# Performance work log

Hardware: AMD Instinct MI355X
Metric: run time of the kernel (lower is better)

## Reference

```python
import jax, jax.numpy as jnp
import numpy as np


def setup_inputs() -> dict:
    key = jax.random.key(0)
    kq, kk, kv = jax.random.split(key, 3)
    B, H, S, D = 2, 8, 2048, 64
    Q = jax.random.normal(kq, (B, H, S, D), dtype=jnp.float32)
    K = jax.random.normal(kk, (B, 1, S, D), dtype=jnp.float32)
    V = jax.random.normal(kv, (B, 1, S, D), dtype=jnp.float32)
    return {"Q": Q, "K": K, "V": V}


def reference(Q, K, V):
    # Multi-query attention: K/V have a single shared head.
    D = Q.shape[-1]
    scale = 1.0 / jnp.sqrt(jnp.asarray(D, dtype=Q.dtype))
    Kh = K[:, 0]  # [B, S, D]
    Vh = V[:, 0]  # [B, S, D]
    # scores: [B, H, Sq, Sk]
    scores = jnp.einsum('bhqd,bkd->bhqk', Q, Kh) * scale
    probs = jax.nn.softmax(scores, axis=-1)
    out = jnp.einsum('bhqk,bkd->bhqd', probs, Vh)  # [B, H, S, D]
    return out
```

## Files before the change

kernel.cpp:

```cpp
#include <hip/hip_runtime.h>
#include <hip/hip_bf16.h>
#include <stdint.h>

typedef __attribute__((ext_vector_type(8)))  short    bf16x8;
typedef __attribute__((ext_vector_type(16))) float    f32x16;
typedef __attribute__((ext_vector_type(2)))  float    f32x2;
typedef __attribute__((ext_vector_type(4)))  float    float4v;
typedef __attribute__((ext_vector_type(4)))  unsigned uint4v;
typedef __attribute__((ext_vector_type(2)))  int      int2v;

#define DEVINL static __device__ __forceinline__

#define B_  2
#define H_  8
#define S_  2048
#define D_  64
#define KVB 128
#define NKT (S_ / KVB)

DEVINL unsigned short f2bf(float f) {
  union { float f; unsigned u; } v; v.f = f;
  unsigned r = v.u + 0x7FFFu + ((v.u >> 16) & 1u);
  return (unsigned short)(r >> 16);
}

DEVINL unsigned short bfu(float f) {
  __hip_bfloat16 h = __float2bfloat16(f);
  unsigned short u; __builtin_memcpy(&u, &h, 2); return u;
}

DEVINL unsigned pkcvt(float a, float b) {
  return (unsigned)bfu(a) | ((unsigned)bfu(b) << 16);
}

DEVINL void gload_lds16(const void* g, void* l) {
  __builtin_amdgcn_global_load_lds(
      (const __attribute__((address_space(1))) void*)g,
      (__attribute__((address_space(3))) void*)l, 16, 0, 0);
}

DEVINL bf16x8 frag_from_words(unsigned a, unsigned b, unsigned c, unsigned d) {
  union { unsigned u[4]; bf16x8 v; } x;
  x.u[0] = a; x.u[1] = b; x.u[2] = c; x.u[3] = d;
  return x.v;
}

#define CROW(r, hi) (((r) & 3) + 8 * ((r) >> 2) + 4 * (hi))

__global__ __launch_bounds__(256) void prep_kernel(
    const float* __restrict__ K, const float* __restrict__ V,
    unsigned short* __restrict__ KVf) {
  const int blk = blockIdx.x;
  const int b  = blk >> 5;
  const int kt = (blk >> 1) & 15;
  const int t  = threadIdx.x;
  const int w  = t >> 6, l = t & 63;
  const int lq = l & 31, hi = l >> 5;

  unsigned short* out = KVf + (size_t)(b * 16 + kt) * 16384;

  if ((blk & 1) == 0) {
#pragma unroll
    for (int j = 0; j < 4; ++j) {
      const int fi = w * 4 + j;
      const int kh = fi >> 2, ks = fi & 3;
      const float* src = K + ((size_t)(b * 2048 + kt * 128 + kh * 32 + lq)) * 64 + ks * 16 + hi * 8;
      const float4v x0 = *(const float4v*)(src);
      const float4v x1 = *(const float4v*)(src + 4);
      uint4v o;
      o.x = (unsigned)f2bf(x0.x) | ((unsigned)f2bf(x0.y) << 16);
      o.y = (unsigned)f2bf(x0.z) | ((unsigned)f2bf(x0.w) << 16);
      o.z = (unsigned)f2bf(x1.x) | ((unsigned)f2bf(x1.y) << 16);
      o.w = (unsigned)f2bf(x1.z) | ((unsigned)f2bf(x1.w) << 16);
      *(uint4v*)(out + fi * 512 + l * 8) = o;
    }
  } else {
    __shared__ float Vs[128][65];
#pragma unroll
    for (int rep = 0; rep < 4; ++rep) {
      const int row = rep * 32 + (t >> 3);
      const int col = (t & 7) * 8;
      const float* src = V + ((size_t)(b * 2048 + kt * 128 + row)) * 64 + col;
      const float4v y0 = *(const float4v*)(src);
      const float4v y1 = *(const float4v*)(src + 4);
      Vs[row][col + 0] = y0.x; Vs[row][col + 1] = y0.y;
      Vs[row][col + 2] = y0.z; Vs[row][col + 3] = y0.w;
      Vs[row][col + 4] = y1.x; Vs[row][col + 5] = y1.y;
      Vs[row][col + 6] = y1.z; Vs[row][col + 7] = y1.w;
    }
    __syncthreads();
#pragma unroll
    for (int j = 0; j < 4; ++j) {
      const int fj = w * 4 + j;
      const int kh = fj >> 2, s = (fj >> 1) & 1, nt = fj & 1;
      const int d  = nt * 32 + lq;
      const int k0 = kh * 32 + s * 16 + hi * 8;
      unsigned short o[8];
#pragma unroll
      for (int e = 0; e < 8; ++e) o[e] = f2bf(Vs[k0 + e][d]);
      uint4v wv;
      wv.x = (unsigned)o[0] | ((unsigned)o[1] << 16);
      wv.y = (unsigned)o[2] | ((unsigned)o[3] << 16);
      wv.z = (unsigned)o[4] | ((unsigned)o[5] << 16);
      wv.w = (unsigned)o[6] | ((unsigned)o[7] << 16);
      *(uint4v*)(out + (16 + fj) * 512 + l * 8) = wv;
    }
  }
}

__global__ __launch_bounds__(512, 4) void attn_kernel(
    const float* __restrict__ Q, const unsigned short* __restrict__ KVf,
    float* __restrict__ O) {
  __shared__ __align__(16) unsigned char smem[65536];

  const int bid = blockIdx.x;
  const int b  = bid >> 8;
  const int h  = (bid >> 5) & 7;
  const int qt = bid & 31;

  const int tid  = threadIdx.x;
  const int lane = tid & 63;
  const int wave = tid >> 6;
  const int qg   = wave & 1;
  const int kh   = wave >> 1;
  const int hi   = lane >> 5;
  const int lq   = lane & 31;

  const unsigned char* kp = (const unsigned char*)KVf + (size_t)b * 16 * 32768;

  const float qscale = 0.125f * 1.4426950408889634f;
  const float* qrow = Q + ((size_t)((b * H_ + h) * S_) + (size_t)(qt * 64 + qg * 32 + lq)) * 64;
  bf16x8 qfrag[4];
#pragma unroll
  for (int ks = 0; ks < 4; ++ks) {
    const float* p = qrow + ks * 16 + hi * 8;
    float4v x0 = *(const float4v*)(p);
    float4v x1 = *(const float4v*)(p + 4);
    bf16x8 f;
    f[0] = (short)f2bf(x0.x * qscale); f[1] = (short)f2bf(x0.y * qscale);
    f[2] = (short)f2bf(x0.z * qscale); f[3] = (short)f2bf(x0.w * qscale);
    f[4] = (short)f2bf(x1.x * qscale); f[5] = (short)f2bf(x1.y * qscale);
    f[6] = (short)f2bf(x1.z * qscale); f[7] = (short)f2bf(x1.w * qscale);
    qfrag[ks] = f;
  }

  f32x16 acc0, acc1;
#pragma unroll
  for (int r = 0; r < 16; ++r) { acc0[r] = 0.f; acc1[r] = 0.f; }
  float lrun = 0.f;

#define STAGE(BUF)                                                        \
  do {                                                                    \
    _Pragma("unroll")                                                     \
    for (int j = 0; j < 4; ++j)                                           \
      gload_lds16(kp + j * 8192 + tid * 16,                               \
                  smem + (BUF) * 32768 + j * 8192 + tid * 16);            \
    kp += 32768;                                                          \
  } while (0)

  STAGE(0);

  int buf = 0;
  for (int kt = 0; kt < NKT; ++kt) {
    __syncthreads();

    if (kt + 1 < NKT) STAGE(buf ^ 1);

    const unsigned short* Kt = (const unsigned short*)(smem + buf * 32768) + kh * 2048;
    f32x16 c;
#pragma unroll
    for (int r = 0; r < 16; ++r) c[r] = 0.f;
    __builtin_amdgcn_s_setprio(1);
#pragma unroll
    for (int ks = 0; ks < 4; ++ks) {
      const bf16x8 a = *(const bf16x8*)(Kt + ks * 512 + lane * 8);
      c = __builtin_amdgcn_mfma_f32_32x32x16_bf16(a, qfrag[ks], c, 0, 0, 0);
    }
    __builtin_amdgcn_s_setprio(0);

#pragma unroll
    for (int r = 0; r < 16; ++r) c[r] = __builtin_amdgcn_exp2f(c[r]);
    f32x2 ps = (f32x2){0.f, 0.f};
#pragma unroll
    for (int r = 0; r < 8; ++r) ps += (f32x2){c[2 * r], c[2 * r + 1]};
    lrun += ps.x + ps.y;

    const unsigned short* Vt = (const unsigned short*)(smem + buf * 32768) + 8192 + kh * 2048;
#pragma unroll
    for (int s = 0; s < 2; ++s) {
      const unsigned wx0 = pkcvt(c[8 * s + 0], c[8 * s + 1]);
      const unsigned wx1 = pkcvt(c[8 * s + 2], c[8 * s + 3]);
      const unsigned wy0 = pkcvt(c[8 * s + 4], c[8 * s + 5]);
      const unsigned wy1 = pkcvt(c[8 * s + 6], c[8 * s + 7]);
      const int2v s02 = __builtin_amdgcn_permlane32_swap((int)wx0, (int)wy0, false, false);
      const int2v s13 = __builtin_amdgcn_permlane32_swap((int)wx1, (int)wy1, false, false);
      const bf16x8 pfrag = frag_from_words((unsigned)s02.x, (unsigned)s13.x,
                                           (unsigned)s02.y, (unsigned)s13.y);
      __builtin_amdgcn_s_setprio(1);
      const bf16x8 bv0 = *(const bf16x8*)(Vt + (s * 2 + 0) * 512 + lane * 8);
      acc0 = __builtin_amdgcn_mfma_f32_32x32x16_bf16(pfrag, bv0, acc0, 0, 0, 0);
      const bf16x8 bv1 = *(const bf16x8*)(Vt + (s * 2 + 1) * 512 + lane * 8);
      acc1 = __builtin_amdgcn_mfma_f32_32x32x16_bf16(pfrag, bv1, acc1, 0, 0, 0);
      __builtin_amdgcn_s_setprio(0);
    }

    buf ^= 1;
  }

  const float lfull = lrun + __shfl_xor(lrun, 32);
  __syncthreads();
  float* Lb = (float*)smem;
  float* Ab = Lb + 256;
  if (lane < 32) Lb[(qg * 4 + kh) * 32 + lane] = lfull;
  __syncthreads();
  const float ltot = Lb[(qg * 4 + 0) * 32 + lq] + Lb[(qg * 4 + 1) * 32 + lq]
                   + Lb[(qg * 4 + 2) * 32 + lq] + Lb[(qg * 4 + 3) * 32 + lq];

  if (kh > 0) {
    float* dst = Ab + (size_t)(qg * 3 + (kh - 1)) * 2048;
#pragma unroll
    for (int r = 0; r < 16; ++r) {
      dst[CROW(r, hi) * 64 + lq]      = acc0[r];
      dst[CROW(r, hi) * 64 + 32 + lq] = acc1[r];
    }
  }
  __syncthreads();
  if (kh == 0) {
    const float linv = 1.f / ltot;
    const float* a0 = Ab + (size_t)(qg * 3 + 0) * 2048;
    const float* a1 = Ab + (size_t)(qg * 3 + 1) * 2048;
    const float* a2 = Ab + (size_t)(qg * 3 + 2) * 2048;
    float* obase = O + ((size_t)((b * H_ + h) * S_) + (size_t)(qt * 64 + qg * 32)) * 64;
#pragma unroll
    for (int r = 0; r < 16; ++r) {
      const float iv = __shfl(linv, CROW(r, hi));
      const int row  = CROW(r, hi);
      obase[(size_t)row * 64 + lq] =
          (acc0[r] + a0[row * 64 + lq] + a1[row * 64 + lq] + a2[row * 64 + lq]) * iv;
      obase[(size_t)row * 64 + 32 + lq] =
          (acc1[r] + a0[row * 64 + 32 + lq] + a1[row * 64 + 32 + lq] + a2[row * 64 + 32 + lq]) * iv;
    }
  }
}

extern "C" void kernel_launch(void* const* d_in, const int* in_sizes, int n_in,
                              void* d_out, int out_size, void* d_ws, size_t ws_size,
                              hipStream_t stream) {
  const float* Q = (const float*)d_in[0];
  const float* K = (const float*)d_in[1];
  const float* V = (const float*)d_in[2];
  float* O = (float*)d_out;

  unsigned short* KVf = (unsigned short*)d_ws;

  prep_kernel<<<64, 256, 0, stream>>>(K, V, KVf);
  attn_kernel<<<B_ * H_ * (S_ / 64), 512, 0, stream>>>(Q, KVf, O);
}
```

Measured before the change: 38.57 us.

## Use 4 waves per block, each handling both query groups, with barrier-free per-wave staging

Cuts the block from 8 waves to 4. Each wave now computes both 32-row query groups against its own K/V slice, so every K and V fragment read from LDS is reused for two MFMA chains. Each wave stages only its own slice of LDS via direct global-to-LDS loads and waits with vmcnt instead of a block-wide __syncthreads per tile, which removes per-iteration barriers. In exchange each wave holds twice the accumulators and Q fragments, which raises register pressure, and there are fewer waves per block to hide latency.

Result: no change. 39.25 us (+1.8%).

```diff
diff --git a/kernel.cpp b/kernel.cpp
--- a/kernel.cpp
+++ b/kernel.cpp
@@ -108,7 +108,7 @@
   }
 }
 
-__global__ __launch_bounds__(512, 4) void attn_kernel(
+__global__ __launch_bounds__(256, 2) void attn_kernel(
     const float* __restrict__ Q, const unsigned short* __restrict__ KVf,
     float* __restrict__ O) {
   __shared__ __align__(16) unsigned char smem[65536];
@@ -120,125 +120,178 @@
 
   const int tid  = threadIdx.x;
   const int lane = tid & 63;
-  const int wave = tid >> 6;
-  const int qg   = wave & 1;
-  const int kh   = wave >> 1;
+  const int kh   = tid >> 6;
   const int hi   = lane >> 5;
   const int lq   = lane & 31;
 
-  const unsigned char* kp = (const unsigned char*)KVf + (size_t)b * 16 * 32768;
+  const unsigned char* wsrc = (const unsigned char*)KVf
+      + (size_t)b * 16 * 32768 + (size_t)kh * 4096 + (size_t)lane * 16;
+  unsigned char* wdst = smem + (size_t)kh * 4096 + (size_t)lane * 16;
 
   const float qscale = 0.125f * 1.4426950408889634f;
-  const float* qrow = Q + ((size_t)((b * H_ + h) * S_) + (size_t)(qt * 64 + qg * 32 + lq)) * 64;
-  bf16x8 qfrag[4];
-#pragma unroll
-  for (int ks = 0; ks < 4; ++ks) {
-    const float* p = qrow + ks * 16 + hi * 8;
-    float4v x0 = *(const float4v*)(p);
-    float4v x1 = *(const float4v*)(p + 4);
-    bf16x8 f;
-    f[0] = (short)f2bf(x0.x * qscale); f[1] = (short)f2bf(x0.y * qscale);
-    f[2] = (short)f2bf(x0.z * qscale); f[3] = (short)f2bf(x0.w * qscale);
-    f[4] = (short)f2bf(x1.x * qscale); f[5] = (short)f2bf(x1.y * qscale);
-    f[6] = (short)f2bf(x1.z * qscale); f[7] = (short)f2bf(x1.w * qscale);
-    qfrag[ks] = f;
-  }
-
-  f32x16 acc0, acc1;
-#pragma unroll
-  for (int r = 0; r < 16; ++r) { acc0[r] = 0.f; acc1[r] = 0.f; }
-  float lrun = 0.f;
-
-#define STAGE(BUF)                                                        \
-  do {                                                                    \
-    _Pragma("unroll")                                                     \
-    for (int j = 0; j < 4; ++j)                                           \
-      gload_lds16(kp + j * 8192 + tid * 16,                               \
-                  smem + (BUF) * 32768 + j * 8192 + tid * 16);            \
-    kp += 32768;                                                          \
+  bf16x8 qfrag0[4], qfrag1[4];
+#pragma unroll
+  for (int qg = 0; qg < 2; ++qg) {
+    const float* qrow = Q + ((size_t)((b * H_ + h) * S_) + (size_t)(qt * 64 + qg * 32 + lq)) * 64;
+#pragma unroll
+    for (int ks = 0; ks < 4; ++ks) {
+      const float* p = qrow + ks * 16 + hi * 8;
+      float4v x0 = *(const float4v*)(p);
+      float4v x1 = *(const float4v*)(p + 4);
+      bf16x8 f;
+      f[0] = (short)f2bf(x0.x * qscale); f[1] = (short)f2bf(x0.y * qscale);
+      f[2] = (short)f2bf(x0.z * qscale); f[3] = (short)f2bf(x0.w * qscale);
+      f[4] = (short)f2bf(x1.x * qscale); f[5] = (short)f2bf(x1.y * qscale);
+      f[6] = (short)f2bf(x1.z * qscale); f[7] = (short)f2bf(x1.w * qscale);
+      if (qg == 0) qfrag0[ks] = f; else qfrag1[ks] = f;
+    }
+  }
+
+  f32x16 acc00, acc01, acc10, acc11;
+#pragma unroll
+  for (int r = 0; r < 16; ++r) { acc00[r] = 0.f; acc01[r] = 0.f; acc10[r] = 0.f; acc11[r] = 0.f; }
+  float lrun0 = 0.f, lrun1 = 0.f;
+
+#define STAGE(BUF, KT)                                                             \
+  do {                                                                             \
+    _Pragma("unroll")                                                              \
+    for (int j = 0; j < 4; ++j) {                                                  \
+      gload_lds16(wsrc + (size_t)(KT) * 32768 + j * 1024,                          \
+                  wdst + (BUF) * 32768 + j * 1024);                                \
+      gload_lds16(wsrc + (size_t)(KT) * 32768 + 16384 + j * 1024,                  \
+                  wdst + (BUF) * 32768 + 16384 + j * 1024);                        \
+    }                                                                              \
   } while (0)
 
-  STAGE(0);
+  STAGE(0, 0);
 
   int buf = 0;
   for (int kt = 0; kt < NKT; ++kt) {
-    __syncthreads();
-
-    if (kt + 1 < NKT) STAGE(buf ^ 1);
-
-    const unsigned short* Kt = (const unsigned short*)(smem + buf * 32768) + kh * 2048;
-    f32x16 c;
-#pragma unroll
-    for (int r = 0; r < 16; ++r) c[r] = 0.f;
+    asm volatile("s_waitcnt vmcnt(0)" ::: "memory");
+    __builtin_amdgcn_sched_barrier(0);
+
+    if (kt + 1 < NKT) STAGE(buf ^ 1, kt + 1);
+
+    const unsigned short* Kt = (const unsigned short*)(smem + buf * 32768 + kh * 4096);
+    f32x16 c0, c1;
+#pragma unroll
+    for (int r = 0; r < 16; ++r) { c0[r] = 0.f; c1[r] = 0.f; }
     __builtin_amdgcn_s_setprio(1);
 #pragma unroll
     for (int ks = 0; ks < 4; ++ks) {
       const bf16x8 a = *(const bf16x8*)(Kt + ks * 512 + lane * 8);
-      c = __builtin_amdgcn_mfma_f32_32x32x16_bf16(a, qfrag[ks], c, 0, 0, 0);
+      c0 = __builtin_amdgcn_mfma_f32_32x32x16_bf16(a, qfrag0[ks], c0, 0, 0, 0);
+      c1 = __builtin_amdgcn_mfma_f32_32x32x16_bf16(a, qfrag1[ks], c1, 0, 0, 0);
     }
     __builtin_amdgcn_s_setprio(0);
 
-#pragma unroll
-    for (int r = 0; r < 16; ++r) c[r] = __builtin_amdgcn_exp2f(c[r]);
-    f32x2 ps = (f32x2){0.f, 0.f};
-#pragma unroll
-    for (int r = 0; r < 8; ++r) ps += (f32x2){c[2 * r], c[2 * r + 1]};
-    lrun += ps.x + ps.y;
-
-    const unsigned short* Vt = (const unsigned short*)(smem + buf * 32768) + 8192 + kh * 2048;
-#pragma unroll
-    for (int s = 0; s < 2; ++s) {
-      const unsigned wx0 = pkcvt(c[8 * s + 0], c[8 * s + 1]);
-      const unsigned wx1 = pkcvt(c[8 * s + 2], c[8 * s + 3]);
-      const unsigned wy0 = pkcvt(c[8 * s + 4], c[8 * s + 5]);
-      const unsigned wy1 = pkcvt(c[8 * s + 6], c[8 * s + 7]);
-      const int2v s02 = __builtin_amdgcn_permlane32_swap((int)wx0, (int)wy0, false, false);
-      const int2v s13 = __builtin_amdgcn_permlane32_swap((int)wx1, (int)wy1, false, false);
-      const bf16x8 pfrag = frag_from_words((unsigned)s02.x, (unsigned)s13.x,
-                                           (unsigned)s02.y, (unsigned)s13.y);
+    const unsigned short* Vt = (const unsigned short*)(smem + buf * 32768 + 16384 + kh * 4096);
+    const bf16x8 v0 = *(const bf16x8*)(Vt + 0 * 512 + lane * 8);
+    const bf16x8 v1 = *(const bf16x8*)(Vt + 1 * 512 + lane * 8);
+    const bf16x8 v2 = *(const bf16x8*)(Vt + 2 * 512 + lane * 8);
+    const bf16x8 v3 = *(const bf16x8*)(Vt + 3 * 512 + lane * 8);
+
+#pragma unroll
+    for (int r = 0; r < 16; ++r) c0[r] = __builtin_amdgcn_exp2f(c0[r]);
+    {
+      f32x2 ps = (f32x2){0.f, 0.f};
+#pragma unroll
+      for (int r = 0; r < 8; ++r) ps += (f32x2){c0[2 * r], c0[2 * r + 1]};
+      lrun0 += ps.x + ps.y;
+      const unsigned wa0 = pkcvt(c0[0], c0[1]),  wa1 = pkcvt(c0[2], c0[3]);
+      const unsigned wa2 = pkcvt(c0[4], c0[5]),  wa3 = pkcvt(c0[6], c0[7]);
+      const unsigned wb0 = pkcvt(c0[8], c0[9]),  wb1 = pkcvt(c0[10], c0[11]);
+      const unsigned wb2 = pkcvt(c0[12], c0[13]), wb3 = pkcvt(c0[14], c0[15]);
+      const int2v a02 = __builtin_amdgcn_permlane32_swap((int)wa0, (int)wa2, false, false);
+      const int2v a13 = __builtin_amdgcn_permlane32_swap((int)wa1, (int)wa3, false, false);
+      const int2v b02 = __builtin_amdgcn_permlane32_swap((int)wb0, (int)wb2, false, false);
+      const int2v b13 = __builtin_amdgcn_permlane32_swap((int)wb1, (int)wb3, false, false);
+      const bf16x8 pf0 = frag_from_words((unsigned)a02.x, (unsigned)a13.x,
+                                         (unsigned)a02.y, (unsigned)a13.y);
+      const bf16x8 pf1 = frag_from_words((unsigned)b02.x, (unsigned)b13.x,
+                                         (unsigned)b02.y, (unsigned)b13.y);
       __builtin_amdgcn_s_setprio(1);
-      const bf16x8 bv0 = *(const bf16x8*)(Vt + (s * 2 + 0) * 512 + lane * 8);
-      acc0 = __builtin_amdgcn_mfma_f32_32x32x16_bf16(pfrag, bv0, acc0, 0, 0, 0);
-      const bf16x8 bv1 = *(const bf16x8*)(Vt + (s * 2 + 1) * 512 + lane * 8);
-      acc1 = __builtin_amdgcn_mfma_f32_32x32x16_bf16(pfrag, bv1, acc1, 0, 0, 0);
+      acc00 = __builtin_amdgcn_mfma_f32_32x32x16_bf16(pf0, v0, acc00, 0, 0, 0);
+      acc01 = __builtin_amdgcn_mfma_f32_32x32x16_bf16(pf0, v1, acc01, 0, 0, 0);
+      acc00 = __builtin_amdgcn_mfma_f32_32x32x16_bf16(pf1, v2, acc00, 0, 0, 0);
+      acc01 = __builtin_amdgcn_mfma_f32_32x32x16_bf16(pf1, v3, acc01, 0, 0, 0);
       __builtin_amdgcn_s_setprio(0);
     }
 
+#pragma unroll
+    for (int r = 0; r < 16; ++r) c1[r] = __builtin_amdgcn_exp2f(c1[r]);
+    {
+      f32x2 ps = (f32x2){0.f, 0.f};
+#pragma unroll
+      for (int r = 0; r < 8; ++r) ps += (f32x2){c1[2 * r], c1[2 * r + 1]};
+      lrun1 += ps.x + ps.y;
+      const unsigned wa0 = pkcvt(c1[0], c1[1]),  wa1 = pkcvt(c1[2], c1[3]);
+      const unsigned wa2 = pkcvt(c1[4], c1[5]),  wa3 = pkcvt(c1[6], c1[7]);
+      const unsigned wb0 = pkcvt(c1[8], c1[9]),  wb1 = pkcvt(c1[10], c1[11]);
+      const unsigned wb2 = pkcvt(c1[12], c1[13]), wb3 = pkcvt(c1[14], c1[15]);
+      const int2v a02 = __builtin_amdgcn_permlane32_swap((int)wa0, (int)wa2, false, false);
+      const int2v a13 = __builtin_amdgcn_permlane32_swap((int)wa1, (int)wa3, false, false);
+      const int2v b02 = __builtin_amdgcn_permlane32_swap((int)wb0, (int)wb2, false, false);
+      const int2v b13 = __builtin_amdgcn_permlane32_swap((int)wb1, (int)wb3, false, false);
+      const bf16x8 pf0 = frag_from_words((unsigned)a02.x, (unsigned)a13.x,
+                                         (unsigned)a02.y, (unsigned)a13.y);
+      const bf16x8 pf1 = frag_from_words((unsigned)b02.x, (unsigned)b13.x,
+                                         (unsigned)b02.y, (unsigned)b13.y);
+      __builtin_amdgcn_s_setprio(1);
+      acc10 = __builtin_amdgcn_mfma_f32_32x32x16_bf16(pf0, v0, acc10, 0, 0, 0);
+      acc11 = __builtin_amdgcn_mfma_f32_32x32x16_bf16(pf0, v1, acc11, 0, 0, 0);
+      acc10 = __builtin_amdgcn_mfma_f32_32x32x16_bf16(pf1, v2, acc10, 0, 0, 0);
+      acc11 = __builtin_amdgcn_mfma_f32_32x32x16_bf16(pf1, v3, acc11, 0, 0, 0);
+      __builtin_amdgcn_s_setprio(0);
+    }
+
     buf ^= 1;
   }
 
-  const float lfull = lrun + __shfl_xor(lrun, 32);
+  const float lfull0 = lrun0 + __shfl_xor(lrun0, 32);
+  const float lfull1 = lrun1 + __shfl_xor(lrun1, 32);
   __syncthreads();
   float* Lb = (float*)smem;
   float* Ab = Lb + 256;
-  if (lane < 32) Lb[(qg * 4 + kh) * 32 + lane] = lfull;
-  __syncthreads();
-  const float ltot = Lb[(qg * 4 + 0) * 32 + lq] + Lb[(qg * 4 + 1) * 32 + lq]
-                   + Lb[(qg * 4 + 2) * 32 + lq] + Lb[(qg * 4 + 3) * 32 + lq];
-
+  if (lane < 32) {
+    Lb[(0 * 4 + kh) * 32 + lane] = lfull0;
+    Lb[(1 * 4 + kh) * 32 + lane] = lfull1;
+  }
   if (kh > 0) {
-    float* dst = Ab + (size_t)(qg * 3 + (kh - 1)) * 2048;
+    float* dst = Ab + (size_t)((kh - 1) * 2) * 2048;
 #pragma unroll
     for (int r = 0; r < 16; ++r) {
-      dst[CROW(r, hi) * 64 + lq]      = acc0[r];
-      dst[CROW(r, hi) * 64 + 32 + lq] = acc1[r];
+      const int row = CROW(r, hi);
+      dst[row * 64 + lq]             = acc00[r];
+      dst[row * 64 + 32 + lq]        = acc01[r];
+      dst[2048 + row * 64 + lq]      = acc10[r];
+      dst[2048 + row * 64 + 32 + lq] = acc11[r];
     }
   }
   __syncthreads();
   if (kh == 0) {
-    const float linv = 1.f / ltot;
-    const float* a0 = Ab + (size_t)(qg * 3 + 0) * 2048;
-    const float* a1 = Ab + (size_t)(qg * 3 + 1) * 2048;
-    const float* a2 = Ab + (size_t)(qg * 3 + 2) * 2048;
-    float* obase = O + ((size_t)((b * H_ + h) * S_) + (size_t)(qt * 64 + qg * 32)) * 64;
+    const float lt0 = Lb[(0 * 4 + 0) * 32 + lq] + Lb[(0 * 4 + 1) * 32 + lq]
+                    + Lb[(0 * 4 + 2) * 32 + lq] + Lb[(0 * 4 + 3) * 32 + lq];
+    const float lt1 = Lb[(1 * 4 + 0) * 32 + lq] + Lb[(1 * 4 + 1) * 32 + lq]
+                    + Lb[(1 * 4 + 2) * 32 + lq] + Lb[(1 * 4 + 3) * 32 + lq];
+    const float li0 = 1.f / lt0, li1 = 1.f / lt1;
+    float* ob0 = O + ((size_t)((b * H_ + h) * S_) + (size_t)(qt * 64)) * 64;
+    float* ob1 = ob0 + (size_t)32 * 64;
 #pragma unroll
     for (int r = 0; r < 16; ++r) {
-      const float iv = __shfl(linv, CROW(r, hi));
-      const int row  = CROW(r, hi);
-      obase[(size_t)row * 64 + lq] =
-          (acc0[r] + a0[row * 64 + lq] + a1[row * 64 + lq] + a2[row * 64 + lq]) * iv;
-      obase[(size_t)row * 64 + 32 + lq] =
-          (acc1[r] + a0[row * 64 + 32 + lq] + a1[row * 64 + 32 + lq] + a2[row * 64 + 32 + lq]) * iv;
+      const int row = CROW(r, hi);
+      const float iv0 = __shfl(li0, row);
+      const float iv1 = __shfl(li1, row);
+      const float* A0 = Ab + row * 64;
+      ob0[(size_t)row * 64 + lq] =
+          (acc00[r] + A0[lq] + A0[2 * 2048 + lq] + A0[4 * 2048 + lq]) * iv0;
+      ob0[(size_t)row * 64 + 32 + lq] =
+          (acc01[r] + A0[32 + lq] + A0[2 * 2048 + 32 + lq] + A0[4 * 2048 + 32 + lq]) * iv0;
+      const float* A1 = A0 + 2048;
+      ob1[(size_t)row * 64 + lq] =
+          (acc10[r] + A1[lq] + A1[2 * 2048 + lq] + A1[4 * 2048 + lq]) * iv1;
+      ob1[(size_t)row * 64 + 32 + lq] =
+          (acc11[r] + A1[32 + lq] + A1[2 * 2048 + 32 + lq] + A1[4 * 2048 + 32 + lq]) * iv1;
     }
   }
 }
@@ -254,5 +307,5 @@
   unsigned short* KVf = (unsigned short*)d_ws;
 
   prep_kernel<<<64, 256, 0, stream>>>(K, V, KVf);
-  attn_kernel<<<B_ * H_ * (S_ / 64), 512, 0, stream>>>(Q, KVf, O);
-}
+  attn_kernel<<<B_ * H_ * (S_ / 64), 256, 0, stream>>>(Q, KVf, O);
+}
```

## Split attention blocks to 32 queries, load V directly to registers, drop per-tile barrier

Applied to the files above, without the earlier changes.

Each block now handles 32 query rows with 4 waves instead of 64 rows with 8. Only K is staged into LDS, and each wave stages and reads only its own slice, so the per-iteration __syncthreads is replaced by a vmcnt wait. V fragments are loaded straight from global memory into registers, which halves shared memory use and removes block-wide synchronisation. The cost is twice as many blocks that each re-read K/V, plus reliance on exact vmcnt counting for correctness.

Result: slower. 40.15 us (+4.1%).

```diff
diff --git a/kernel.cpp b/kernel.cpp
--- a/kernel.cpp
+++ b/kernel.cpp
@@ -108,28 +108,29 @@
   }
 }
 
-__global__ __launch_bounds__(512, 4) void attn_kernel(
+__global__ __launch_bounds__(256, 4) void attn_kernel(
     const float* __restrict__ Q, const unsigned short* __restrict__ KVf,
     float* __restrict__ O) {
-  __shared__ __align__(16) unsigned char smem[65536];
+  __shared__ __align__(16) unsigned char smem[32768];
 
   const int bid = blockIdx.x;
-  const int b  = bid >> 8;
-  const int h  = (bid >> 5) & 7;
-  const int qt = bid & 31;
+  const int b  = bid >> 9;
+  const int h  = (bid >> 6) & 7;
+  const int qt = bid & 63;
 
   const int tid  = threadIdx.x;
   const int lane = tid & 63;
-  const int wave = tid >> 6;
-  const int qg   = wave & 1;
-  const int kh   = wave >> 1;
+  const int kh   = tid >> 6;
   const int hi   = lane >> 5;
   const int lq   = lane & 31;
 
-  const unsigned char* kp = (const unsigned char*)KVf + (size_t)b * 16 * 32768;
+  const unsigned char* ksrc = (const unsigned char*)KVf
+      + (size_t)b * 524288 + (size_t)kh * 4096 + (size_t)lane * 16;
+  const unsigned char* vp = ksrc + 16384;
+  unsigned char* wdst = smem + (size_t)kh * 4096 + (size_t)lane * 16;
 
   const float qscale = 0.125f * 1.4426950408889634f;
-  const float* qrow = Q + ((size_t)((b * H_ + h) * S_) + (size_t)(qt * 64 + qg * 32 + lq)) * 64;
+  const float* qrow = Q + ((size_t)((b * H_ + h) * S_) + (size_t)(qt * 32 + lq)) * 64;
   bf16x8 qfrag[4];
 #pragma unroll
   for (int ks = 0; ks < 4; ++ks) {
@@ -149,24 +150,29 @@
   for (int r = 0; r < 16; ++r) { acc0[r] = 0.f; acc1[r] = 0.f; }
   float lrun = 0.f;
 
-#define STAGE(BUF)                                                        \
-  do {                                                                    \
-    _Pragma("unroll")                                                     \
-    for (int j = 0; j < 4; ++j)                                           \
-      gload_lds16(kp + j * 8192 + tid * 16,                               \
-                  smem + (BUF) * 32768 + j * 8192 + tid * 16);            \
-    kp += 32768;                                                          \
-  } while (0)
-
-  STAGE(0);
+#pragma unroll
+  for (int j = 0; j < 4; ++j) gload_lds16(ksrc + j * 1024, wdst + j * 1024);
+  const unsigned char* kp = ksrc + 32768;
 
   int buf = 0;
   for (int kt = 0; kt < NKT; ++kt) {
-    __syncthreads();
-
-    if (kt + 1 < NKT) STAGE(buf ^ 1);
-
-    const unsigned short* Kt = (const unsigned short*)(smem + buf * 32768) + kh * 2048;
+    const bf16x8 v0 = *(const bf16x8*)(vp);
+    const bf16x8 v1 = *(const bf16x8*)(vp + 1024);
+    const bf16x8 v2 = *(const bf16x8*)(vp + 2048);
+    const bf16x8 v3 = *(const bf16x8*)(vp + 3072);
+    vp += 32768;
+
+    asm volatile("s_waitcnt vmcnt(4)" ::: "memory");
+    __builtin_amdgcn_sched_barrier(0);
+
+    if (kt + 1 < NKT) {
+#pragma unroll
+      for (int j = 0; j < 4; ++j)
+        gload_lds16(kp + j * 1024, smem + (buf ^ 1) * 16384 + kh * 4096 + lane * 16 + j * 1024);
+      kp += 32768;
+    }
+
+    const unsigned short* Kt = (const unsigned short*)(smem + buf * 16384 + kh * 4096);
     f32x16 c;
 #pragma unroll
     for (int r = 0; r < 16; ++r) c[r] = 0.f;
@@ -185,24 +191,25 @@
     for (int r = 0; r < 8; ++r) ps += (f32x2){c[2 * r], c[2 * r + 1]};
     lrun += ps.x + ps.y;
 
-    const unsigned short* Vt = (const unsigned short*)(smem + buf * 32768) + 8192 + kh * 2048;
-#pragma unroll
-    for (int s = 0; s < 2; ++s) {
-      const unsigned wx0 = pkcvt(c[8 * s + 0], c[8 * s + 1]);
-      const unsigned wx1 = pkcvt(c[8 * s + 2], c[8 * s + 3]);
-      const unsigned wy0 = pkcvt(c[8 * s + 4], c[8 * s + 5]);
-      const unsigned wy1 = pkcvt(c[8 * s + 6], c[8 * s + 7]);
-      const int2v s02 = __builtin_amdgcn_permlane32_swap((int)wx0, (int)wy0, false, false);
-      const int2v s13 = __builtin_amdgcn_permlane32_swap((int)wx1, (int)wy1, false, false);
-      const bf16x8 pfrag = frag_from_words((unsigned)s02.x, (unsigned)s13.x,
-                                           (unsigned)s02.y, (unsigned)s13.y);
-      __builtin_amdgcn_s_setprio(1);
-      const bf16x8 bv0 = *(const bf16x8*)(Vt + (s * 2 + 0) * 512 + lane * 8);
-      acc0 = __builtin_amdgcn_mfma_f32_32x32x16_bf16(pfrag, bv0, acc0, 0, 0, 0);
-      const bf16x8 bv1 = *(const bf16x8*)(Vt + (s * 2 + 1) * 512 + lane * 8);
-      acc1 = __builtin_amdgcn_mfma_f32_32x32x16_bf16(pfrag, bv1, acc1, 0, 0, 0);
-      __builtin_amdgcn_s_setprio(0);
-    }
+    const unsigned wa0 = pkcvt(c[0], c[1]),   wa1 = pkcvt(c[2], c[3]);
+    const unsigned wa2 = pkcvt(c[4], c[5]),   wa3 = pkcvt(c[6], c[7]);
+    const unsigned wb0 = pkcvt(c[8], c[9]),   wb1 = pkcvt(c[10], c[11]);
+    const unsigned wb2 = pkcvt(c[12], c[13]), wb3 = pkcvt(c[14], c[15]);
+    const int2v a02 = __builtin_amdgcn_permlane32_swap((int)wa0, (int)wa2, false, false);
+    const int2v a13 = __builtin_amdgcn_permlane32_swap((int)wa1, (int)wa3, false, false);
+    const int2v b02 = __builtin_amdgcn_permlane32_swap((int)wb0, (int)wb2, false, false);
+    const int2v b13 = __builtin_amdgcn_permlane32_swap((int)wb1, (int)wb3, false, false);
+    const bf16x8 pf0 = frag_from_words((unsigned)a02.x, (unsigned)a13.x,
+                                       (unsigned)a02.y, (unsigned)a13.y);
+    const bf16x8 pf1 = frag_from_words((unsigned)b02.x, (unsigned)b13.x,
+                                       (unsigned)b02.y, (unsigned)b13.y);
+
+    __builtin_amdgcn_s_setprio(1);
+    acc0 = __builtin_amdgcn_mfma_f32_32x32x16_bf16(pf0, v0, acc0, 0, 0, 0);
+    acc1 = __builtin_amdgcn_mfma_f32_32x32x16_bf16(pf0, v1, acc1, 0, 0, 0);
+    acc0 = __builtin_amdgcn_mfma_f32_32x32x16_bf16(pf1, v2, acc0, 0, 0, 0);
+    acc1 = __builtin_amdgcn_mfma_f32_32x32x16_bf16(pf1, v3, acc1, 0, 0, 0);
+    __builtin_amdgcn_s_setprio(0);
 
     buf ^= 1;
   }
@@ -210,35 +217,31 @@
   const float lfull = lrun + __shfl_xor(lrun, 32);
   __syncthreads();
   float* Lb = (float*)smem;
-  float* Ab = Lb + 256;
-  if (lane < 32) Lb[(qg * 4 + kh) * 32 + lane] = lfull;
-  __syncthreads();
-  const float ltot = Lb[(qg * 4 + 0) * 32 + lq] + Lb[(qg * 4 + 1) * 32 + lq]
-                   + Lb[(qg * 4 + 2) * 32 + lq] + Lb[(qg * 4 + 3) * 32 + lq];
-
+  float* Ab = Lb + 128;
+  if (lane < 32) Lb[kh * 32 + lane] = lfull;
   if (kh > 0) {
-    float* dst = Ab + (size_t)(qg * 3 + (kh - 1)) * 2048;
+    float* dst = Ab + (size_t)(kh - 1) * 2048;
 #pragma unroll
     for (int r = 0; r < 16; ++r) {
-      dst[CROW(r, hi) * 64 + lq]      = acc0[r];
-      dst[CROW(r, hi) * 64 + 32 + lq] = acc1[r];
+      const int row = CROW(r, hi);
+      dst[row * 64 + lq]      = acc0[r];
+      dst[row * 64 + 32 + lq] = acc1[r];
     }
   }
   __syncthreads();
   if (kh == 0) {
+    const float ltot = Lb[lq] + Lb[32 + lq] + Lb[64 + lq] + Lb[96 + lq];
     const float linv = 1.f / ltot;
-    const float* a0 = Ab + (size_t)(qg * 3 + 0) * 2048;
-    const float* a1 = Ab + (size_t)(qg * 3 + 1) * 2048;
-    const float* a2 = Ab + (size_t)(qg * 3 + 2) * 2048;
-    float* obase = O + ((size_t)((b * H_ + h) * S_) + (size_t)(qt * 64 + qg * 32)) * 64;
+    float* obase = O + ((size_t)((b * H_ + h) * S_) + (size_t)(qt * 32)) * 64;
 #pragma unroll
     for (int r = 0; r < 16; ++r) {
-      const float iv = __shfl(linv, CROW(r, hi));
-      const int row  = CROW(r, hi);
+      const int row = CROW(r, hi);
+      const float iv = __shfl(linv, row);
+      const float* A = Ab + row * 64;
       obase[(size_t)row * 64 + lq] =
-          (acc0[r] + a0[row * 64 + lq] + a1[row * 64 + lq] + a2[row * 64 + lq]) * iv;
+          (acc0[r] + A[lq] + A[2048 + lq] + A[4096 + lq]) * iv;
       obase[(size_t)row * 64 + 32 + lq] =
-          (acc1[r] + a0[row * 64 + 32 + lq] + a1[row * 64 + 32 + lq] + a2[row * 64 + 32 + lq]) * iv;
+          (acc1[r] + A[32 + lq] + A[2048 + 32 + lq] + A[4096 + 32 + lq]) * iv;
     }
   }
 }
@@ -254,5 +257,5 @@
   unsigned short* KVf = (unsigned short*)d_ws;
 
   prep_kernel<<<64, 256, 0, stream>>>(K, V, KVf);
-  attn_kernel<<<B_ * H_ * (S_ / 64), 512, 0, stream>>>(Q, KVf, O);
-}
+  attn_kernel<<<B_ * H_ * (S_ / 32), 256, 0, stream>>>(Q, KVf, O);
+}
```
